# Performance work log

Measured on AMD Instinct MI355X. Metric: run time of the kernel, lower is better.

The kernel has to match this reference:

```python
import jax, jax.numpy as jnp
import numpy as np

DIM = 1280
NUM_HEADS = 16
HEAD_DIM = DIM // NUM_HEADS  # 80
SCALE = HEAD_DIM ** -0.5
N_CHUNKS = 4
CHUNK = 2048
TOTAL = N_CHUNKS * CHUNK  # 8192


def setup_inputs() -> dict:
    key = jax.random.key(0)
    ks = jax.random.split(key, 5)
    hidden_states = jax.random.normal(ks[0], (TOTAL, DIM), dtype=jnp.float32)
    cu_seqlens = (jnp.arange(N_CHUNKS + 1, dtype=jnp.int32) * CHUNK)
    qkv_w = jax.random.normal(ks[1], (3 * DIM, DIM), dtype=jnp.float32) * (DIM ** -0.5)
    qkv_b = jax.random.normal(ks[2], (3 * DIM,), dtype=jnp.float32) * 0.02
    proj_w = jax.random.normal(ks[3], (DIM, DIM), dtype=jnp.float32) * (DIM ** -0.5)
    proj_b = jax.random.normal(ks[4], (DIM,), dtype=jnp.float32) * 0.02
    return {"hidden_states": hidden_states, "cu_seqlens": cu_seqlens,
            "qkv_w": qkv_w, "qkv_b": qkv_b, "proj_w": proj_w, "proj_b": proj_b}


def reference(hidden_states, cu_seqlens, qkv_w, qkv_b, proj_w, proj_b):
    S = hidden_states.shape[0]
    # fused QKV projection: (S, 3*dim) -> q,k,v each (S, H, Dh)
    qkv = hidden_states @ qkv_w.T + qkv_b
    qkv = qkv.reshape(S, 3, NUM_HEADS, HEAD_DIM)
    q, k, v = qkv[:, 0], qkv[:, 1], qkv[:, 2]
    # chunk boundaries are static metadata (module calls .tolist() on them)
    cu = np.asarray(cu_seqlens)
    outs = []
    for s, e in zip(cu[:-1], cu[1:]):
        s, e = int(s), int(e)
        qc = q[s:e].transpose(1, 0, 2)  # (H, L, Dh)
        kc = k[s:e].transpose(1, 0, 2)
        vc = v[s:e].transpose(1, 0, 2)
        # full (non-causal) attention within the chunk; softmax in fp32
        logits = jnp.einsum('hqd,hkd->hqk', qc, kc) * SCALE
        w = jax.nn.softmax(logits.astype(jnp.float32), axis=-1).astype(qc.dtype)
        oc = jnp.einsum('hqk,hkd->hqd', w, vc)  # (H, L, Dh)
        outs.append(oc.transpose(1, 0, 2).reshape(e - s, DIM))
    attn_out = jnp.concatenate(outs, axis=0)  # (S, dim)
    return attn_out @ proj_w.T + proj_b
```

## Files before the change

kernel.cpp:

```cpp
#include <hip/hip_runtime.h>
#include <hip/hip_bf16.h>
#include <stdint.h>

#define NHEADS 16
#define HDIM 80
#define CHUNK 2048
#define QSCALE 0.11180339887498949f
#define L2E 1.4426950408889634f

typedef __bf16 bf16x8 __attribute__((ext_vector_type(8)));
typedef float f32x4 __attribute__((ext_vector_type(4)));

__device__ __forceinline__ unsigned short f2bf(float f) {
  union { float f; unsigned u; } x; x.f = f;
  unsigned r = (x.u + 0x7fffu + ((x.u >> 16) & 1u)) >> 16;
  return (unsigned short)r;
}

__device__ __forceinline__ float fexp2(float x) {
  float r;
  asm("v_exp_f32 %0, %1" : "=v"(r) : "v"(x));
  return r;
}

__device__ __forceinline__ void gload16(const void* g, void* lds) {
  __builtin_amdgcn_global_load_lds((const __attribute__((address_space(1))) void*)g,
                                   (__attribute__((address_space(3))) void*)lds, 16, 0, 0);
}

__global__ __launch_bounds__(256) void cvt3_f32_bf16(
    const float* __restrict__ a, unsigned short* __restrict__ ao, int na4,
    const float* __restrict__ b, unsigned short* __restrict__ bo, int nb4,
    const float* __restrict__ c, unsigned short* __restrict__ co, int nc4) {
  const int stride = gridDim.x * 256;
  for (int i = blockIdx.x * 256 + threadIdx.x; i < na4; i += stride) {
    float4 v = reinterpret_cast<const float4*>(a)[i];
    ushort4 o; o.x = f2bf(v.x); o.y = f2bf(v.y); o.z = f2bf(v.z); o.w = f2bf(v.w);
    reinterpret_cast<ushort4*>(ao)[i] = o;
  }
  for (int i = blockIdx.x * 256 + threadIdx.x; i < nb4; i += stride) {
    float4 v = reinterpret_cast<const float4*>(b)[i];
    ushort4 o; o.x = f2bf(v.x); o.y = f2bf(v.y); o.z = f2bf(v.z); o.w = f2bf(v.w);
    reinterpret_cast<ushort4*>(bo)[i] = o;
  }
  for (int i = blockIdx.x * 256 + threadIdx.x; i < nc4; i += stride) {
    float4 v = reinterpret_cast<const float4*>(c)[i];
    ushort4 o; o.x = f2bf(v.x); o.y = f2bf(v.y); o.z = f2bf(v.z); o.w = f2bf(v.w);
    reinterpret_cast<ushort4*>(co)[i] = o;
  }
}

__global__ __launch_bounds__(256) void gemm_bt(
    const unsigned short* __restrict__ A, const unsigned short* __restrict__ B,
    const float* __restrict__ bias, unsigned short* __restrict__ C,
    float* __restrict__ Cf, unsigned short* __restrict__ vt,
    int M, int N, int K, int lda, int scaleN, float scaleVal)
{
  __shared__ unsigned short Ash[128 * 64];
  __shared__ unsigned short Bsh[128 * 64];
  const int tid = threadIdx.x;
  const int lane = tid & 63;
  const int w = tid >> 6;
  const int wr = w >> 1, wc = w & 1;
  const int l15 = lane & 15, lq = lane >> 4;
  const long bm = (long)blockIdx.y * 128;
  const long bn = (long)blockIdx.x * 128;

  f32x4 acc[4][4];
#pragma unroll
  for (int i = 0; i < 4; i++)
#pragma unroll
    for (int j = 0; j < 4; j++) acc[i][j] = f32x4{0.f, 0.f, 0.f, 0.f};

  const int rlo = lane >> 3;
  const int sg  = (lane & 7) ^ rlo;

  for (long k0 = 0; k0 < K; k0 += 64) {
    __syncthreads();
#pragma unroll
    for (int j = 0; j < 4; j++) {
      int c = w * 4 + j;
      gload16(A + (bm + c * 8 + rlo) * (long)lda + k0 + sg * 8,
              (char*)Ash + c * 1024);
      gload16(B + (bn + c * 8 + rlo) * (long)K + k0 + sg * 8,
              (char*)Bsh + c * 1024);
    }
    __syncthreads();
#pragma unroll
    for (int kk = 0; kk < 2; kk++) {
      const int so = (((kk * 4 + lq) ^ (l15 & 7))) * 8;
      bf16x8 af[4], bfr[4];
#pragma unroll
      for (int x = 0; x < 4; x++) {
        af[x]  = *reinterpret_cast<const bf16x8*>(Ash + (wr * 64 + x * 16 + l15) * 64 + so);
        bfr[x] = *reinterpret_cast<const bf16x8*>(Bsh + (wc * 64 + x * 16 + l15) * 64 + so);
      }
#pragma unroll
      for (int x = 0; x < 4; x++)
#pragma unroll
        for (int y = 0; y < 4; y++)
          acc[x][y] = __builtin_amdgcn_mfma_f32_16x16x32_bf16(af[x], bfr[y], acc[x][y], 0, 0, 0);
    }
  }

#pragma unroll
  for (int x = 0; x < 4; x++) {
    long row0 = bm + wr * 64 + x * 16 + lq * 4;
#pragma unroll
    for (int y = 0; y < 4; y++) {
      int colu = (int)bn + wc * 64 + y * 16;
      int col = colu + l15;
      float bs = bias[col];
      if (vt != nullptr && colu >= 2560) {
        int vcol = col - 2560;
        int vh = vcol / 80, vd = vcol % 80;
        int chp = ((int)(row0 >> 11)) * 16 + vh;
        int seq = (int)row0 & 2047;
        ushort4 o;
        o.x = f2bf(acc[x][y][0] + bs);
        o.y = f2bf(acc[x][y][1] + bs);
        o.z = f2bf(acc[x][y][2] + bs);
        o.w = f2bf(acc[x][y][3] + bs);
        *reinterpret_cast<ushort4*>(vt + ((size_t)chp * 80 + vd) * 2048 + seq) = o;
      } else {
        float sc = (col < scaleN) ? scaleVal : 1.0f;
        if (Cf != nullptr) {
#pragma unroll
          for (int r = 0; r < 4; r++)
            Cf[(size_t)(row0 + r) * N + col] = (acc[x][y][r] + bs) * sc;
        } else {
#pragma unroll
          for (int r = 0; r < 4; r++)
            C[(size_t)(row0 + r) * N + col] = f2bf((acc[x][y][r] + bs) * sc);
        }
      }
    }
  }
}

__global__ __launch_bounds__(256, 3) void attn_kernel(
    const unsigned short* __restrict__ qkv, const unsigned short* __restrict__ vt,
    unsigned short* __restrict__ outq)
{
  __shared__ char Kbuf[10240];
  __shared__ char Vbuf[12288];
  __shared__ unsigned short Psh[4][32 * 72];

  const int tid = threadIdx.x;
  const int lane = tid & 63;
  const int w = tid >> 6;
  const int l15 = lane & 15, lq = lane >> 4;

  const int b = blockIdx.x;
  const int qt = (b >> 3) & 15;
  const int chp = (b & 7) * 8 + (b >> 7);
  const int ch = chp >> 4;
  const int head = chp & 15;

  const size_t rs = 3840;
  const unsigned short* qbase = qkv + (size_t)(ch * CHUNK) * rs + head * HDIM;
  const char* kbase = (const char*)(qbase + 1280);
  const char* vbase = (const char*)(vt + (size_t)chp * HDIM * 2048);

  int kgo[3]; bool kact[3];
  const int koff0 = w * 1024;
#pragma unroll
  for (int j = 0; j < 3; j++) {
    int c = w + 4 * j;
    kact[j] = (c < 10);
    int cc = kact[j] ? c : 0;
    int s = cc * 64 + lane;
    kgo[j] = (s / 10) * 7680 + (s % 10) * 16;
  }
  int vgo[3];
  const int vw = (w + 2) & 3;
#pragma unroll
  for (int j = 0; j < 3; j++) {
    int c = vw + 4 * j;
    int s2 = c * 64 + lane;
    if (s2 > 719) s2 = 719;
    int d = s2 / 9, u = s2 % 9;
    int ue = (u == 8) ? 0 : u;
    vgo[j] = d * 4096 + ue * 16;
  }

  const int qr0 = qt * 128 + w * 32;
  bf16x8 qa[2][2], qa2[2];
#pragma unroll
  for (int qf = 0; qf < 2; qf++) {
    const unsigned short* qrow = qbase + (size_t)(qr0 + qf * 16 + l15) * rs;
    qa[qf][0] = *reinterpret_cast<const bf16x8*>(qrow + lq * 8);
    qa[qf][1] = *reinterpret_cast<const bf16x8*>(qrow + 32 + lq * 8);
    if (lq < 2) qa2[qf] = *reinterpret_cast<const bf16x8*>(qrow + 64 + lq * 8);
    else        qa2[qf] = bf16x8{};
  }

  bf16x8 onesb;
  {
    __bf16 o = (l15 == 0) ? (__bf16)1.0f : (__bf16)0.0f;
    onesb = bf16x8{o, o, o, o, o, o, o, o};
  }

  f32x4 acc[2][6];
#pragma unroll
  for (int qf = 0; qf < 2; qf++)
#pragma unroll
    for (int df = 0; df < 6; df++) acc[qf][df] = f32x4{0.f, 0.f, 0.f, 0.f};
  float mst[2][4];
#pragma unroll
  for (int qf = 0; qf < 2; qf++)
#pragma unroll
    for (int r = 0; r < 4; r++) mst[qf][r] = 16.0f;

#pragma unroll
  for (int j = 0; j < 3; j++)
    if (kact[j]) gload16(kbase + kgo[j], Kbuf + koff0 + j * 4096);
#pragma unroll
  for (int j = 0; j < 3; j++) gload16(vbase + vgo[j], Vbuf + vw * 1024 + j * 4096);
  __syncthreads();

  for (int kt = 0; kt < CHUNK; kt += 64) {
    float tmax[2][4];
#pragma unroll
    for (int qf = 0; qf < 2; qf++)
#pragma unroll
      for (int r = 0; r < 4; r++) tmax[qf][r] = -1e30f;

    const unsigned short* Ksh = (const unsigned short*)Kbuf;
#pragma unroll
    for (int kf = 0; kf < 4; kf++) {
      const unsigned short* kr = Ksh + (kf * 16 + l15) * 80;
      bf16x8 kb0 = *reinterpret_cast<const bf16x8*>(kr + lq * 8);
      bf16x8 kb1 = *reinterpret_cast<const bf16x8*>(kr + 32 + lq * 8);
      bf16x8 kb2 = (lq < 2) ? *reinterpret_cast<const bf16x8*>(kr + 64 + lq * 8) : bf16x8{};
#pragma unroll
      for (int qf = 0; qf < 2; qf++) {
        f32x4 sv = f32x4{0.f, 0.f, 0.f, 0.f};
        sv = __builtin_amdgcn_mfma_f32_16x16x32_bf16(qa[qf][0], kb0, sv, 0, 0, 0);
        sv = __builtin_amdgcn_mfma_f32_16x16x32_bf16(qa[qf][1], kb1, sv, 0, 0, 0);
        sv = __builtin_amdgcn_mfma_f32_16x16x32_bf16(qa2[qf], kb2, sv, 0, 0, 0);
#pragma unroll
        for (int r = 0; r < 4; r++) {
          tmax[qf][r] = fmaxf(tmax[qf][r], sv[r]);
          float p = fexp2((sv[r] - mst[qf][r]) * L2E);
          unsigned pk;
          asm("v_cvt_pk_bf16_f32 %0, %1, %2" : "=v"(pk) : "v"(p), "v"(p));
          Psh[w][(qf * 16 + lq * 4 + r) * 72 + kf * 16 + l15] = (unsigned short)pk;
        }
      }
    }

    bool need = false;
#pragma unroll
    for (int qf = 0; qf < 2; qf++)
#pragma unroll
      for (int r = 0; r < 4; r++)
        need = need || (tmax[qf][r] > mst[qf][r] + 8.0f);
    const bool resc = __any(need);
    float alpha[2][4];
    if (resc) {
#pragma unroll
      for (int m = 1; m < 16; m <<= 1)
#pragma unroll
        for (int qf = 0; qf < 2; qf++)
#pragma unroll
          for (int r = 0; r < 4; r++)
            tmax[qf][r] = fmaxf(tmax[qf][r], __shfl_xor(tmax[qf][r], m, 64));
#pragma unroll
      for (int qf = 0; qf < 2; qf++)
#pragma unroll
        for (int r = 0; r < 4; r++) {
          float mnew = fmaxf(mst[qf][r], tmax[qf][r]);
          alpha[qf][r] = fexp2((mst[qf][r] - mnew) * L2E);
          mst[qf][r] = mnew;
        }
    }

    __syncthreads();

    if (kt + 64 < CHUNK) {
      const int ktB = (kt + 64) * 7680;
#pragma unroll
      for (int j = 0; j < 3; j++)
        if (kact[j]) gload16(kbase + kgo[j] + ktB, Kbuf + koff0 + j * 4096);
    }

    const unsigned short* Vsh = (const unsigned short*)Vbuf;
#pragma unroll
    for (int ks = 0; ks < 2; ks++) {
      bf16x8 pa[2];
#pragma unroll
      for (int qf = 0; qf < 2; qf++)
        pa[qf] = *reinterpret_cast<const bf16x8*>(&Psh[w][(qf * 16 + l15) * 72 + ks * 32 + lq * 8]);
#pragma unroll
      for (int df = 0; df < 5; df++) {
        bf16x8 vb = *reinterpret_cast<const bf16x8*>(&Vsh[(df * 16 + l15) * 72 + ks * 32 + lq * 8]);
#pragma unroll
        for (int qf = 0; qf < 2; qf++)
          acc[qf][df] = __builtin_amdgcn_mfma_f32_16x16x32_bf16(pa[qf], vb, acc[qf][df], 0, 0, 0);
      }
#pragma unroll
      for (int qf = 0; qf < 2; qf++)
        acc[qf][5] = __builtin_amdgcn_mfma_f32_16x16x32_bf16(pa[qf], onesb, acc[qf][5], 0, 0, 0);
    }

    if (resc) {
#pragma unroll
      for (int qf = 0; qf < 2; qf++)
#pragma unroll
        for (int df = 0; df < 6; df++)
#pragma unroll
          for (int r = 0; r < 4; r++) acc[qf][df][r] *= alpha[qf][r];
    }

    __syncthreads();

    if (kt + 64 < CHUNK) {
      const int ktV = (kt + 64) * 2;
#pragma unroll
      for (int j = 0; j < 3; j++)
        gload16(vbase + vgo[j] + ktV, Vbuf + vw * 1024 + j * 4096);
    }
  }

  unsigned short* obase = outq + (size_t)(ch * CHUNK) * rs + head * HDIM;
#pragma unroll
  for (int qf = 0; qf < 2; qf++) {
    float inv[4];
#pragma unroll
    for (int r = 0; r < 4; r++) inv[r] = 1.0f / __shfl(acc[qf][5][r], lq * 16, 64);
#pragma unroll
    for (int df = 0; df < 5; df++) {
      int col = df * 16 + l15;
#pragma unroll
      for (int r = 0; r < 4; r++) {
        float v = acc[qf][df][r] * inv[r];
        obase[(size_t)(qr0 + qf * 16 + lq * 4 + r) * rs + col] = f2bf(v);
      }
    }
  }
}

extern "C" void kernel_launch(void* const* d_in, const int* in_sizes, int n_in,
                              void* d_out, int out_size, void* d_ws, size_t ws_size,
                              hipStream_t stream) {
  const float* hs    = (const float*)d_in[0];
  const float* qkvw  = (const float*)d_in[2];
  const float* qkvb  = (const float*)d_in[3];
  const float* projw = (const float*)d_in[4];
  const float* projb = (const float*)d_in[5];

  char* ws = (char*)d_ws;
  unsigned short* hs_bf    = (unsigned short*)ws;
  unsigned short* qkvw_bf  = (unsigned short*)(ws + 20971520);
  unsigned short* projw_bf = (unsigned short*)(ws + 20971520 + 9830400);
  unsigned short* qkv_bf   = (unsigned short*)(ws + 20971520 + 9830400 + 3276800);
  unsigned short* vT = (unsigned short*)d_out;

  cvt3_f32_bf16<<<2048, 256, 0, stream>>>(hs, hs_bf, 8192 * 1280 / 4,
                                          qkvw, qkvw_bf, 3840 * 1280 / 4,
                                          projw, projw_bf, 1280 * 1280 / 4);

  gemm_bt<<<dim3(30, 64), 256, 0, stream>>>(hs_bf, qkvw_bf, qkvb, qkv_bf, nullptr, vT,
                                            8192, 3840, 1280, 1280, 1280, QSCALE);
  attn_kernel<<<dim3(1024), 256, 0, stream>>>(qkv_bf, vT, qkv_bf);
  gemm_bt<<<dim3(10, 64), 256, 0, stream>>>(qkv_bf, projw_bf, projb,
                                            nullptr, (float*)d_out, nullptr,
                                            8192, 1280, 1280, 3840, 0, 1.0f);
}
```

Before: 294.7 us.

## Keep softmax probabilities in registers via transposed QK MFMA, drop P LDS round-trip

Swaps the MFMA operand order so S^T comes out with each lane holding four consecutive keys for one query. The probabilities can then be packed straight into the A-operand layout of the PV MFMA, which removes the per-warp P shared-memory buffer and its scalar stores and reloads. Row-max tracking becomes one value per lane per fragment, reduced with two shuffles, and the rescale factors are redistributed by shuffle. The V reads are split into two 8-byte LDS loads to match the new key permutation, which adds LDS instructions.

```diff
diff --git a/kernel.cpp b/kernel.cpp
--- a/kernel.cpp
+++ b/kernel.cpp
@@ -20,6 +20,12 @@
 __device__ __forceinline__ float fexp2(float x) {
   float r;
   asm("v_exp_f32 %0, %1" : "=v"(r) : "v"(x));
+  return r;
+}
+
+__device__ __forceinline__ unsigned cvtpk(float lo, float hi) {
+  unsigned r;
+  asm("v_cvt_pk_bf16_f32 %0, %1, %2" : "=v"(r) : "v"(lo), "v"(hi));
   return r;
 }
 
@@ -144,7 +150,6 @@
 {
   __shared__ char Kbuf[10240];
   __shared__ char Vbuf[12288];
-  __shared__ unsigned short Psh[4][32 * 72];
 
   const int tid = threadIdx.x;
   const int lane = tid & 63;
@@ -206,11 +211,8 @@
   for (int qf = 0; qf < 2; qf++)
 #pragma unroll
     for (int df = 0; df < 6; df++) acc[qf][df] = f32x4{0.f, 0.f, 0.f, 0.f};
-  float mst[2][4];
-#pragma unroll
-  for (int qf = 0; qf < 2; qf++)
-#pragma unroll
-    for (int r = 0; r < 4; r++) mst[qf][r] = 16.0f;
+  float mst[2];
+  mst[0] = 16.0f; mst[1] = 16.0f;
 
 #pragma unroll
   for (int j = 0; j < 3; j++)
@@ -220,11 +222,8 @@
   __syncthreads();
 
   for (int kt = 0; kt < CHUNK; kt += 64) {
-    float tmax[2][4];
-#pragma unroll
-    for (int qf = 0; qf < 2; qf++)
-#pragma unroll
-      for (int r = 0; r < 4; r++) tmax[qf][r] = -1e30f;
+    float tmax[2] = {-1e30f, -1e30f};
+    union { unsigned u[4]; bf16x8 v; } paq[2][2];
 
     const unsigned short* Ksh = (const unsigned short*)Kbuf;
 #pragma unroll
@@ -236,44 +235,35 @@
 #pragma unroll
       for (int qf = 0; qf < 2; qf++) {
         f32x4 sv = f32x4{0.f, 0.f, 0.f, 0.f};
-        sv = __builtin_amdgcn_mfma_f32_16x16x32_bf16(qa[qf][0], kb0, sv, 0, 0, 0);
-        sv = __builtin_amdgcn_mfma_f32_16x16x32_bf16(qa[qf][1], kb1, sv, 0, 0, 0);
-        sv = __builtin_amdgcn_mfma_f32_16x16x32_bf16(qa2[qf], kb2, sv, 0, 0, 0);
-#pragma unroll
-        for (int r = 0; r < 4; r++) {
-          tmax[qf][r] = fmaxf(tmax[qf][r], sv[r]);
-          float p = fexp2((sv[r] - mst[qf][r]) * L2E);
-          unsigned pk;
-          asm("v_cvt_pk_bf16_f32 %0, %1, %2" : "=v"(pk) : "v"(p), "v"(p));
-          Psh[w][(qf * 16 + lq * 4 + r) * 72 + kf * 16 + l15] = (unsigned short)pk;
-        }
-      }
-    }
-
-    bool need = false;
-#pragma unroll
-    for (int qf = 0; qf < 2; qf++)
-#pragma unroll
-      for (int r = 0; r < 4; r++)
-        need = need || (tmax[qf][r] > mst[qf][r] + 8.0f);
-    const bool resc = __any(need);
-    float alpha[2][4];
+        sv = __builtin_amdgcn_mfma_f32_16x16x32_bf16(kb0, qa[qf][0], sv, 0, 0, 0);
+        sv = __builtin_amdgcn_mfma_f32_16x16x32_bf16(kb1, qa[qf][1], sv, 0, 0, 0);
+        sv = __builtin_amdgcn_mfma_f32_16x16x32_bf16(kb2, qa2[qf], sv, 0, 0, 0);
+        tmax[qf] = fmaxf(tmax[qf],
+                         fmaxf(fmaxf(sv[0], sv[1]), fmaxf(sv[2], sv[3])));
+        float p0 = fexp2((sv[0] - mst[qf]) * L2E);
+        float p1 = fexp2((sv[1] - mst[qf]) * L2E);
+        float p2 = fexp2((sv[2] - mst[qf]) * L2E);
+        float p3 = fexp2((sv[3] - mst[qf]) * L2E);
+        paq[qf][kf >> 1].u[(kf & 1) * 2]     = cvtpk(p0, p1);
+        paq[qf][kf >> 1].u[(kf & 1) * 2 + 1] = cvtpk(p2, p3);
+      }
+    }
+
+    const bool resc = __any((tmax[0] > mst[0] + 8.0f) || (tmax[1] > mst[1] + 8.0f));
+    float alpha_acc[2][4];
     if (resc) {
 #pragma unroll
-      for (int m = 1; m < 16; m <<= 1)
-#pragma unroll
-        for (int qf = 0; qf < 2; qf++)
-#pragma unroll
-          for (int r = 0; r < 4; r++)
-            tmax[qf][r] = fmaxf(tmax[qf][r], __shfl_xor(tmax[qf][r], m, 64));
-#pragma unroll
-      for (int qf = 0; qf < 2; qf++)
-#pragma unroll
-        for (int r = 0; r < 4; r++) {
-          float mnew = fmaxf(mst[qf][r], tmax[qf][r]);
-          alpha[qf][r] = fexp2((mst[qf][r] - mnew) * L2E);
-          mst[qf][r] = mnew;
-        }
+      for (int qf = 0; qf < 2; qf++) {
+        float t = tmax[qf];
+        t = fmaxf(t, __shfl_xor(t, 16, 64));
+        t = fmaxf(t, __shfl_xor(t, 32, 64));
+        float mnew = fmaxf(mst[qf], t);
+        float a_s = fexp2((mst[qf] - mnew) * L2E);
+        mst[qf] = mnew;
+#pragma unroll
+        for (int r = 0; r < 4; r++)
+          alpha_acc[qf][r] = __shfl(a_s, lq * 4 + r, 64);
+      }
     }
 
     __syncthreads();
@@ -288,29 +278,28 @@
     const unsigned short* Vsh = (const unsigned short*)Vbuf;
 #pragma unroll
     for (int ks = 0; ks < 2; ks++) {
-      bf16x8 pa[2];
+#pragma unroll
+      for (int df = 0; df < 5; df++) {
+        const unsigned short* vp = Vsh + (df * 16 + l15) * 72 + ks * 32 + lq * 4;
+        union { unsigned u[4]; bf16x8 v; } vb;
+        *reinterpret_cast<uint2*>(&vb.u[0]) = *reinterpret_cast<const uint2*>(vp);
+        *reinterpret_cast<uint2*>(&vb.u[2]) = *reinterpret_cast<const uint2*>(vp + 16);
+#pragma unroll
+        for (int qf = 0; qf < 2; qf++)
+          acc[qf][df] = __builtin_amdgcn_mfma_f32_16x16x32_bf16(paq[qf][ks].v, vb.v, acc[qf][df], 0, 0, 0);
+      }
 #pragma unroll
       for (int qf = 0; qf < 2; qf++)
-        pa[qf] = *reinterpret_cast<const bf16x8*>(&Psh[w][(qf * 16 + l15) * 72 + ks * 32 + lq * 8]);
-#pragma unroll
-      for (int df = 0; df < 5; df++) {
-        bf16x8 vb = *reinterpret_cast<const bf16x8*>(&Vsh[(df * 16 + l15) * 72 + ks * 32 + lq * 8]);
-#pragma unroll
-        for (int qf = 0; qf < 2; qf++)
-          acc[qf][df] = __builtin_amdgcn_mfma_f32_16x16x32_bf16(pa[qf], vb, acc[qf][df], 0, 0, 0);
-      }
+        acc[qf][5] = __builtin_amdgcn_mfma_f32_16x16x32_bf16(paq[qf][ks].v, onesb, acc[qf][5], 0, 0, 0);
+    }
+
+    if (resc) {
 #pragma unroll
       for (int qf = 0; qf < 2; qf++)
-        acc[qf][5] = __builtin_amdgcn_mfma_f32_16x16x32_bf16(pa[qf], onesb, acc[qf][5], 0, 0, 0);
-    }
-
-    if (resc) {
-#pragma unroll
-      for (int qf = 0; qf < 2; qf++)
 #pragma unroll
         for (int df = 0; df < 6; df++)
 #pragma unroll
-          for (int r = 0; r < 4; r++) acc[qf][df][r] *= alpha[qf][r];
+          for (int r = 0; r < 4; r++) acc[qf][df][r] *= alpha_acc[qf][r];
     }
 
     __syncthreads();
```

Result: faster. 278.7 us (median of 2 runs) (-5.4%).
